# Performance work log

Measured on AMD Instinct MI355X. Metric: run time of the kernel, lower is better.

Reference implementation:

```python
import jax, jax.numpy as jnp
import numpy as np

B, S, IN_F, OUT_F = 4, 2048, 4096, 4096
ALPHA = 0.01

def setup_inputs() -> dict:
    key = jax.random.key(0)
    k1, k2 = jax.random.split(key, 2)
    # int8-valued activations and weights (stored as int32 per harness dtype)
    x = jax.random.randint(k1, (B, S, IN_F), -127, 127, dtype=jnp.int32)
    weight = jax.random.randint(k2, (IN_F, OUT_F), -127, 127, dtype=jnp.int32)
    bias = jnp.zeros((1, OUT_F), dtype=jnp.float16)
    alpha = jnp.full((1,), ALPHA, dtype=jnp.float32)
    return {"x": x, "weight": weight, "bias": bias, "alpha": alpha}

def reference(x, weight, bias, alpha):
    # Faithful to forward's default (non-hybrid) path:
    # y = F.linear(x.float(), weight.t().float(), bias.float()) * alpha
    # F.linear(x, W^T) == x @ W, with W shape (in_features, out_features).
    x_shape = x.shape
    xf = x.reshape(-1, x_shape[-1]).astype(jnp.float32)          # [B*S, in]
    wf = weight.astype(jnp.float32)                               # [in, out]
    y = (xf @ wf + bias.astype(jnp.float32)) * alpha              # [B*S, out]
    return y.reshape(*x_shape[:-1], -1)                           # [B, S, out]
```

## Files before the change

kernel.cpp:

```cpp
#include <hip/hip_runtime.h>
#include <hip/hip_fp16.h>

using i32x4  = __attribute__((ext_vector_type(4)))  int;
using i32x16 = __attribute__((ext_vector_type(16))) int;

static constexpr int M  = 4 * 2048;
static constexpr int N  = 4096;
static constexpr int K  = 4096;
static constexpr int NT = K / 64;
static constexpr int TILE = 128 * 64;

static constexpr int PX_BLOCKS = (int)((size_t)M * K / 16 / 256);
static constexpr int PW_BLOCKS = (int)((size_t)N * K / 16 / 256);

__device__ __forceinline__ unsigned pack4(i32x4 v) {
  return (unsigned)((v.x & 255) | ((v.y & 255) << 8) | ((v.z & 255) << 16) | (v.w << 24));
}

__global__ __launch_bounds__(256) void pack_kernel(const int* __restrict__ x,
                                                   const int* __restrict__ w,
                                                   unsigned char* __restrict__ wa,
                                                   unsigned char* __restrict__ wb) {
  if (blockIdx.x < PX_BLOCKS) {
    unsigned g = blockIdx.x * 256 + threadIdx.x;
    unsigned tile = g >> 9, gt = g & 511;
    unsigned kg = gt >> 7, row = gt & 127;
    unsigned br = tile >> 6, kt = tile & 63;
    const int* src = x + ((size_t)(br * 128 + row) * K + kt * 64 + kg * 16);
    i32x4 v0 = *(const i32x4*)(src + 0);
    i32x4 v1 = *(const i32x4*)(src + 4);
    i32x4 v2 = *(const i32x4*)(src + 8);
    i32x4 v3 = *(const i32x4*)(src + 12);
    i32x4 d;
    d.x = (int)pack4(v0); d.y = (int)pack4(v1); d.z = (int)pack4(v2); d.w = (int)pack4(v3);
    *(i32x4*)(wa + (size_t)g * 16) = d;
  } else {
    unsigned g = (blockIdx.x - PX_BLOCKS) * 256 + threadIdx.x;
    unsigned tile = g >> 9, gt = g & 511;
    unsigned kg = gt >> 7, col = gt & 127;
    unsigned bn = tile >> 6, kt = tile & 63;
    unsigned n  = bn * 128 + col;
    unsigned k0 = kt * 64 + kg * 16;
    const int* src = w + (size_t)k0 * N + n;
    i32x4 d;
#pragma unroll
    for (int j = 0; j < 4; ++j) {
      int b0 = src[(size_t)(j * 4 + 0) * N];
      int b1 = src[(size_t)(j * 4 + 1) * N];
      int b2 = src[(size_t)(j * 4 + 2) * N];
      int b3 = src[(size_t)(j * 4 + 3) * N];
      d[j] = (b0 & 255) | ((b1 & 255) << 8) | ((b2 & 255) << 16) | (b3 << 24);
    }
    *(i32x4*)(wb + (size_t)g * 16) = d;
  }
}


__global__ __launch_bounds__(256, 4) void gemm_i8(const unsigned char* __restrict__ wa,
                                                  const unsigned char* __restrict__ wb,
                                                  const __half* __restrict__ bias,
                                                  const float* __restrict__ alphaP,
                                                  float* __restrict__ out) {
  const int tid  = threadIdx.x;
  const int lane = tid & 63;
  const int w    = tid >> 6;
  const int wr   = w >> 1, wc = w & 1;
  const int l31  = lane & 31;
  const int kgl  = lane >> 5;

  const int bc = blockIdx.x;
  const int br = blockIdx.y;

  const unsigned char* gaw = wa + (size_t)br * NT * TILE;
  const unsigned char* gbw = wb + (size_t)bc * NT * TILE;

  const int aoff = kgl * 2048 + (wr * 64 + l31) * 16;
  const int boff = kgl * 2048 + (wc * 64 + l31) * 16;

  i32x4 a0, a1, b0, b1, c0, c1, d0, d1;

#define LOADT(T) do {                                                \
    const unsigned char* at = gaw + (size_t)(T) * TILE;              \
    const unsigned char* bt = gbw + (size_t)(T) * TILE;              \
    a0 = *(const i32x4*)(at + aoff);                                 \
    a1 = *(const i32x4*)(at + aoff + 512);                           \
    b0 = *(const i32x4*)(bt + boff);                                 \
    b1 = *(const i32x4*)(bt + boff + 512);                           \
    c0 = *(const i32x4*)(at + 4096 + aoff);                          \
    c1 = *(const i32x4*)(at + 4096 + aoff + 512);                    \
    d0 = *(const i32x4*)(bt + 4096 + boff);                          \
    d1 = *(const i32x4*)(bt + 4096 + boff + 512);                    \
  } while (0)

  i32x16 acc[2][2] = {};

#define MF(mi, ni, A, B) \
  acc[mi][ni] = __builtin_amdgcn_mfma_i32_32x32x32_i8(A, B, acc[mi][ni], 0, 0, 0)

  LOADT(0);
  for (int t = 0; t < NT; ++t) {
    MF(0, 0, a0, b0); MF(0, 1, a0, b1);
    MF(1, 0, a1, b0); MF(1, 1, a1, b1);
    MF(0, 0, c0, d0); MF(0, 1, c0, d1);
    MF(1, 0, c1, d0); MF(1, 1, c1, d1);
    if (t + 1 < NT) LOADT(t + 1);
  }

  const float alpha = *alphaP;
  const int row0 = br * 128 + wr * 64 + 4 * kgl;
  const int col0 = bc * 128 + wc * 64 + l31;
#pragma unroll
  for (int ni = 0; ni < 2; ++ni) {
    const int col = col0 + ni * 32;
    const float bf = __half2float(bias[col]);
#pragma unroll
    for (int mi = 0; mi < 2; ++mi) {
#pragma unroll
      for (int r = 0; r < 16; ++r) {
        const int row = row0 + mi * 32 + (r & 3) + 8 * (r >> 2);
        out[(size_t)row * N + col] = ((float)acc[mi][ni][r] + bf) * alpha;
      }
    }
  }
#undef MF
#undef LOADT
}

extern "C" void kernel_launch(void* const* d_in, const int* in_sizes, int n_in,
                              void* d_out, int out_size, void* d_ws, size_t ws_size,
                              hipStream_t stream) {
  const int*    x     = (const int*)d_in[0];
  const int*    wgt   = (const int*)d_in[1];
  const __half* bias  = (const __half*)d_in[2];
  const float*  alpha = (const float*)d_in[3];
  float*        out   = (float*)d_out;

  unsigned char* wa = (unsigned char*)d_ws;
  unsigned char* wb = wa + (size_t)M * K;

  pack_kernel<<<PX_BLOCKS + PW_BLOCKS, 256, 0, stream>>>(x, wgt, wa, wb);

  dim3 grid(N / 128, M / 128);
  gemm_i8<<<grid, 256, 0, stream>>>(wa, wb, bias, alpha, out);
}
```

Baseline: 235.4 us.

## Stage int8 tiles through LDS with triple-buffered async loads and 256x256 blocks

The GEMM stops reading operands straight from global memory into registers. It now uses 256x256 block tiles with 512 threads, copies the packed A and B tiles into a three-stage LDS ring via global_load_lds, and computes with 16x16x64 int8 MFMA. Each phase issues the prefetch for tile t+2, then runs the MFMA cluster with raised wave priority. The larger tile raises operand reuse and cuts global traffic, at the cost of more barriers per K step, 96KB of shared memory and higher accumulator register pressure. The pack kernel layout changes to match the 256-wide tiles.

```diff
diff --git a/kernel.cpp b/kernel.cpp
--- a/kernel.cpp
+++ b/kernel.cpp
@@ -2,13 +2,14 @@
 #include <hip/hip_fp16.h>
 
 using i32x4  = __attribute__((ext_vector_type(4)))  int;
-using i32x16 = __attribute__((ext_vector_type(16))) int;
 
 static constexpr int M  = 4 * 2048;
 static constexpr int N  = 4096;
 static constexpr int K  = 4096;
-static constexpr int NT = K / 64;
-static constexpr int TILE = 128 * 64;
+static constexpr int BK = 64;
+static constexpr int NT = K / BK;
+static constexpr int ATILE = 256 * 64;
+static constexpr int BTILE = 256 * 64;
 
 static constexpr int PX_BLOCKS = (int)((size_t)M * K / 16 / 256);
 static constexpr int PW_BLOCKS = (int)((size_t)N * K / 16 / 256);
@@ -23,10 +24,11 @@
                                                    unsigned char* __restrict__ wb) {
   if (blockIdx.x < PX_BLOCKS) {
     unsigned g = blockIdx.x * 256 + threadIdx.x;
-    unsigned tile = g >> 9, gt = g & 511;
-    unsigned kg = gt >> 7, row = gt & 127;
-    unsigned br = tile >> 6, kt = tile & 63;
-    const int* src = x + ((size_t)(br * 128 + row) * K + kt * 64 + kg * 16);
+    unsigned row = g & 255;
+    unsigned kg  = (g >> 8) & 3;
+    unsigned kt  = (g >> 10) & 63;
+    unsigned br  = g >> 16;
+    const int* src = x + ((size_t)(br * 256 + row) * K + kt * 64 + kg * 16);
     i32x4 v0 = *(const i32x4*)(src + 0);
     i32x4 v1 = *(const i32x4*)(src + 4);
     i32x4 v2 = *(const i32x4*)(src + 8);
@@ -36,11 +38,12 @@
     *(i32x4*)(wa + (size_t)g * 16) = d;
   } else {
     unsigned g = (blockIdx.x - PX_BLOCKS) * 256 + threadIdx.x;
-    unsigned tile = g >> 9, gt = g & 511;
-    unsigned kg = gt >> 7, col = gt & 127;
-    unsigned bn = tile >> 6, kt = tile & 63;
-    unsigned n  = bn * 128 + col;
-    unsigned k0 = kt * 64 + kg * 16;
+    unsigned col = g & 255;
+    unsigned kg  = (g >> 8) & 3;
+    unsigned kt  = (g >> 10) & 63;
+    unsigned bn  = g >> 16;
+    unsigned n   = bn * 256 + col;
+    unsigned k0  = kt * 64 + kg * 16;
     const int* src = w + (size_t)k0 * N + n;
     i32x4 d;
 #pragma unroll
@@ -56,74 +59,112 @@
 }
 
 
-__global__ __launch_bounds__(256, 4) void gemm_i8(const unsigned char* __restrict__ wa,
+__device__ __forceinline__ void gload_lds16(const void* g, void* l) {
+  __builtin_amdgcn_global_load_lds((const __attribute__((address_space(1))) unsigned int*)g,
+                                   (__attribute__((address_space(3))) unsigned int*)l,
+                                   16, 0, 0);
+}
+
+#define FENCE()   asm volatile("" ::: "memory")
+#define BARRIER() do { FENCE(); __builtin_amdgcn_s_barrier(); FENCE(); } while (0)
+#define MFI(A, B, C) __builtin_amdgcn_mfma_i32_16x16x64_i8(A, B, C, 0, 0, 0)
+
+__global__ __launch_bounds__(512, 2) void gemm_i8(const unsigned char* __restrict__ wa,
                                                   const unsigned char* __restrict__ wb,
                                                   const __half* __restrict__ bias,
                                                   const float* __restrict__ alphaP,
                                                   float* __restrict__ out) {
+  __shared__ __align__(16) unsigned char As[3][ATILE];
+  __shared__ __align__(16) unsigned char Bs[3][BTILE];
+
   const int tid  = threadIdx.x;
   const int lane = tid & 63;
   const int w    = tid >> 6;
-  const int wr   = w >> 1, wc = w & 1;
-  const int l31  = lane & 31;
-  const int kgl  = lane >> 5;
+  const int wr   = w >> 2, wc = w & 3;
+  const int l15  = lane & 15;
+  const int kg4096 = (lane >> 4) * 4096;
 
   const int bc = blockIdx.x;
   const int br = blockIdx.y;
 
-  const unsigned char* gaw = wa + (size_t)br * NT * TILE;
-  const unsigned char* gbw = wb + (size_t)bc * NT * TILE;
+  const unsigned char* ga = wa + (size_t)br * NT * ATILE;
+  const unsigned char* gb = wb + (size_t)bc * NT * BTILE;
 
-  const int aoff = kgl * 2048 + (wr * 64 + l31) * 16;
-  const int boff = kgl * 2048 + (wc * 64 + l31) * 16;
-
-  i32x4 a0, a1, b0, b1, c0, c1, d0, d1;
-
-#define LOADT(T) do {                                                \
-    const unsigned char* at = gaw + (size_t)(T) * TILE;              \
-    const unsigned char* bt = gbw + (size_t)(T) * TILE;              \
-    a0 = *(const i32x4*)(at + aoff);                                 \
-    a1 = *(const i32x4*)(at + aoff + 512);                           \
-    b0 = *(const i32x4*)(bt + boff);                                 \
-    b1 = *(const i32x4*)(bt + boff + 512);                           \
-    c0 = *(const i32x4*)(at + 4096 + aoff);                          \
-    c1 = *(const i32x4*)(at + 4096 + aoff + 512);                    \
-    d0 = *(const i32x4*)(bt + 4096 + boff);                          \
-    d1 = *(const i32x4*)(bt + 4096 + boff + 512);                    \
+#define STAGE_Q(BUF, T, QI) do {                                               \
+    const unsigned char* sq_src =                                              \
+        ((QI) < 2 ? ga + (size_t)(T) * ATILE + (QI) * 8192                     \
+                  : gb + (size_t)(T) * BTILE + ((QI) & 1) * 8192)              \
+        + w * 1024 + lane * 16;                                                \
+    unsigned char* sq_dst =                                                    \
+        ((QI) < 2 ? &As[BUF][(QI) * 8192] : &Bs[BUF][((QI) & 1) * 8192])       \
+        + w * 1024;                                                            \
+    gload_lds16(sq_src, sq_dst);                                               \
   } while (0)
 
-  i32x16 acc[2][2] = {};
+  i32x4 acc[8][4] = {};
 
-#define MF(mi, ni, A, B) \
-  acc[mi][ni] = __builtin_amdgcn_mfma_i32_32x32x32_i8(A, B, acc[mi][ni], 0, 0, 0)
+#define PHASE(ASL, BSL, T, PBUF, QR, QC, LAST) do {                            \
+    const unsigned char* Ab = (ASL) + kg4096 + (wr * 128 + (QR) * 64 + l15) * 16; \
+    const unsigned char* Bb = (BSL) + kg4096 + (wc * 64 + (QC) * 32 + l15) * 16;  \
+    i32x4 a0 = *(const i32x4*)(Ab +   0);                                      \
+    i32x4 a1 = *(const i32x4*)(Ab + 256);                                      \
+    i32x4 a2 = *(const i32x4*)(Ab + 512);                                      \
+    i32x4 a3 = *(const i32x4*)(Ab + 768);                                      \
+    i32x4 b0 = *(const i32x4*)(Bb +   0);                                      \
+    i32x4 b1 = *(const i32x4*)(Bb + 256);                                      \
+    if ((T) + 2 < NT) STAGE_Q(PBUF, (T) + 2, (QR) * 2 + (QC));                 \
+    BARRIER();                                                                 \
+    asm volatile("s_waitcnt lgkmcnt(0)" ::: "memory");                         \
+    __builtin_amdgcn_s_setprio(1);                                             \
+    acc[(QR)*4+0][(QC)*2+0] = MFI(a0, b0, acc[(QR)*4+0][(QC)*2+0]);            \
+    acc[(QR)*4+0][(QC)*2+1] = MFI(a0, b1, acc[(QR)*4+0][(QC)*2+1]);            \
+    acc[(QR)*4+1][(QC)*2+0] = MFI(a1, b0, acc[(QR)*4+1][(QC)*2+0]);            \
+    acc[(QR)*4+1][(QC)*2+1] = MFI(a1, b1, acc[(QR)*4+1][(QC)*2+1]);            \
+    acc[(QR)*4+2][(QC)*2+0] = MFI(a2, b0, acc[(QR)*4+2][(QC)*2+0]);            \
+    acc[(QR)*4+2][(QC)*2+1] = MFI(a2, b1, acc[(QR)*4+2][(QC)*2+1]);            \
+    acc[(QR)*4+3][(QC)*2+0] = MFI(a3, b0, acc[(QR)*4+3][(QC)*2+0]);            \
+    acc[(QR)*4+3][(QC)*2+1] = MFI(a3, b1, acc[(QR)*4+3][(QC)*2+1]);            \
+    __builtin_amdgcn_s_setprio(0);                                             \
+    if (LAST) {                                                                \
+      if ((T) + 2 < NT)      asm volatile("s_waitcnt vmcnt(4)" ::: "memory");  \
+      else if ((T) + 1 < NT) asm volatile("s_waitcnt vmcnt(0)" ::: "memory");  \
+    }                                                                          \
+    BARRIER();                                                                 \
+  } while (0)
 
-  LOADT(0);
+  STAGE_Q(0, 0, 0); STAGE_Q(0, 0, 1); STAGE_Q(0, 0, 2); STAGE_Q(0, 0, 3);
+  STAGE_Q(1, 1, 0); STAGE_Q(1, 1, 1); STAGE_Q(1, 1, 2); STAGE_Q(1, 1, 3);
+  asm volatile("s_waitcnt vmcnt(4)" ::: "memory");
+  BARRIER();
+
   for (int t = 0; t < NT; ++t) {
-    MF(0, 0, a0, b0); MF(0, 1, a0, b1);
-    MF(1, 0, a1, b0); MF(1, 1, a1, b1);
-    MF(0, 0, c0, d0); MF(0, 1, c0, d1);
-    MF(1, 0, c1, d0); MF(1, 1, c1, d1);
-    if (t + 1 < NT) LOADT(t + 1);
+    const unsigned char* asl = &As[t % 3][0];
+    const unsigned char* bsl = &Bs[t % 3][0];
+    const int pbuf = (t + 2) % 3;
+    PHASE(asl, bsl, t, pbuf, 0, 0, 0);
+    PHASE(asl, bsl, t, pbuf, 0, 1, 0);
+    PHASE(asl, bsl, t, pbuf, 1, 0, 0);
+    PHASE(asl, bsl, t, pbuf, 1, 1, 1);
   }
 
   const float alpha = *alphaP;
-  const int row0 = br * 128 + wr * 64 + 4 * kgl;
-  const int col0 = bc * 128 + wc * 64 + l31;
+  const int rbase = br * 256 + wr * 128 + (lane >> 4) * 4;
+  const int cbase = bc * 256 + wc * 64 + l15;
 #pragma unroll
-  for (int ni = 0; ni < 2; ++ni) {
-    const int col = col0 + ni * 32;
+  for (int c = 0; c < 4; ++c) {
+    const int col = cbase + c * 16;
     const float bf = __half2float(bias[col]);
 #pragma unroll
-    for (int mi = 0; mi < 2; ++mi) {
+    for (int f = 0; f < 8; ++f) {
 #pragma unroll
-      for (int r = 0; r < 16; ++r) {
-        const int row = row0 + mi * 32 + (r & 3) + 8 * (r >> 2);
-        out[(size_t)row * N + col] = ((float)acc[mi][ni][r] + bf) * alpha;
+      for (int r = 0; r < 4; ++r) {
+        const int row = rbase + f * 16 + r;
+        out[(size_t)row * N + col] = ((float)acc[f][c][r] + bf) * alpha;
       }
     }
   }
-#undef MF
-#undef LOADT
+#undef PHASE
+#undef STAGE_Q
 }
 
 extern "C" void kernel_launch(void* const* d_in, const int* in_sizes, int n_in,
@@ -140,6 +181,6 @@
 
   pack_kernel<<<PX_BLOCKS + PW_BLOCKS, 256, 0, stream>>>(x, wgt, wa, wb);
 
-  dim3 grid(N / 128, M / 128);
-  gemm_i8<<<grid, 256, 0, stream>>>(wa, wb, bias, alpha, out);
+  dim3 grid(N / 256, M / 256);
+  gemm_i8<<<grid, 512, 0, stream>>>(wa, wb, bias, alpha, out);
 }
```

Result: slower. 260.7 us (+10.8%).
